# Kernel optimization log

Measured on AMD Instinct MI355X. Metric: run time of the kernel, lower is better.

## Reference

```python
import jax, jax.numpy as jnp
import numpy as np

D_MODEL = 1024
N_LAYERS = 2
D_STATE = 64
D_CONV = 4
EXPAND = 2
D_INNER = EXPAND * D_MODEL            # 2048
HEADDIM = D_STATE                     # 64 (headdim=d_state per module code)
NHEADS = D_INNER // HEADDIM           # 32
CONV_DIM = D_INNER + 2 * D_STATE      # 2176 (ngroups=1)
D_IN_PROJ = 2 * D_INNER + 2 * D_STATE + NHEADS  # 4256
EPS = 1e-5


def setup_inputs() -> dict:
    key = jax.random.key(0)
    ks = jax.random.split(key, 8)
    B, L = 2, 4096
    return {
        "x": jax.random.normal(ks[0], (B, L, D_MODEL), jnp.float32),
        "ln_w": jnp.ones((N_LAYERS, D_MODEL), jnp.float32),
        "ln_b": jnp.zeros((N_LAYERS, D_MODEL), jnp.float32),
        "in_proj_w": jax.random.normal(ks[1], (N_LAYERS, D_IN_PROJ, D_MODEL), jnp.float32) * (D_MODEL ** -0.5),
        "conv_w": jax.random.normal(ks[2], (N_LAYERS, CONV_DIM, D_CONV), jnp.float32) * (D_CONV ** -0.5),
        "conv_b": jnp.zeros((N_LAYERS, CONV_DIM), jnp.float32),
        "dt_bias": jax.random.normal(ks[3], (N_LAYERS, NHEADS), jnp.float32) * 0.5,
        "A_log": jnp.log(jax.random.uniform(ks[4], (N_LAYERS, NHEADS), jnp.float32, 1.0, 16.0)),
        "D": jnp.ones((N_LAYERS, NHEADS), jnp.float32),
        "rms_w": jnp.ones((N_LAYERS, D_INNER), jnp.float32),
        "out_proj_w": jax.random.normal(ks[5], (N_LAYERS, D_MODEL, D_INNER), jnp.float32) * (D_INNER ** -0.5),
    }


def _layernorm(x, w, b):
    m = x.mean(-1, keepdims=True)
    v = ((x - m) ** 2).mean(-1, keepdims=True)
    return (x - m) * jax.lax.rsqrt(v + EPS) * w + b


def _mamba2(u, in_w, conv_w, conv_b, dt_bias, A_log, Dp, rms_w, out_w):
    b, l, _ = u.shape
    zxbcdt = u @ in_w.T                                   # (b,l,D_IN_PROJ)
    z, xBC, dt = jnp.split(zxbcdt, [D_INNER, D_INNER + CONV_DIM], axis=-1)
    dt = jax.nn.softplus(dt + dt_bias)                    # (b,l,H)
    # causal depthwise conv over sequence
    xBC = jnp.transpose(xBC, (0, 2, 1))                   # (b,C,l)
    xBC = jax.lax.conv_general_dilated(
        xBC, conv_w[:, None, :], (1,), [(D_CONV - 1, 0)],
        dimension_numbers=("NCH", "OIH", "NCH"), feature_group_count=CONV_DIM)
    xBC = jnp.transpose(xBC, (0, 2, 1)) + conv_b
    xBC = jax.nn.silu(xBC)
    xh, Bm, Cm = jnp.split(xBC, [D_INNER, D_INNER + D_STATE], axis=-1)
    xh = xh.reshape(b, l, NHEADS, HEADDIM)                # (b,l,H,P)
    A = -jnp.exp(A_log)                                   # (H,)
    dA = jnp.exp(dt * A)                                  # (b,l,H)

    def step(state, inputs):
        dA_t, dt_t, x_t, B_t, C_t = inputs                # (b,H),(b,H),(b,H,P),(b,N),(b,N)
        state = dA_t[:, :, None, None] * state + (dt_t[:, :, None] * x_t)[..., None] * B_t[:, None, None, :]
        y_t = jnp.einsum("bhpn,bn->bhp", state, C_t)
        return state, y_t

    xs = (jnp.moveaxis(dA, 1, 0), jnp.moveaxis(dt, 1, 0), jnp.moveaxis(xh, 1, 0),
          jnp.moveaxis(Bm, 1, 0), jnp.moveaxis(Cm, 1, 0))
    init = jnp.zeros((b, NHEADS, HEADDIM, D_STATE), u.dtype)
    _, ys = jax.lax.scan(step, init, xs)                  # ys: (l,b,H,P)
    y = jnp.moveaxis(ys, 0, 1) + Dp[None, None, :, None] * xh
    y = y.reshape(b, l, D_INNER)
    # gated RMSNorm (norm_before_gate=False): gate then rmsnorm
    y = y * jax.nn.silu(z)
    y = y * jax.lax.rsqrt(jnp.mean(y * y, -1, keepdims=True) + EPS) * rms_w
    return y @ out_w.T


def reference(x, ln_w, ln_b, in_proj_w, conv_w, conv_b, dt_bias, A_log, D, rms_w, out_proj_w):
    h = x
    for i in range(N_LAYERS):
        res = h
        h = _layernorm(h, ln_w[i], ln_b[i])
        h = _mamba2(h, in_proj_w[i], conv_w[i], conv_b[i], dt_bias[i], A_log[i], D[i], rms_w[i], out_proj_w[i])
        h = h + res
    return h
```

## Files before the change

### kernel.cpp

```cpp
#include <hip/hip_runtime.h>
#include <stdint.h>

#define D_MODEL   1024
#define D_STATE   64
#define D_INNER   2048
#define NHEADS    32
#define CONV_DIM  2176
#define D_IN_PROJ 4256
#define NPAD1     4352
#define LSEQ      4096
#define BL        8192
#define NCHUNK    32
#define TCH       128
#define EPS       1e-5f

typedef __attribute__((ext_vector_type(8))) _Float16 f16x8;
typedef __attribute__((ext_vector_type(4))) _Float16 f16x4;
typedef __attribute__((ext_vector_type(4))) float f32x4;

__device__ __forceinline__ void load_lds16(const void* g, void* l) {
  __builtin_amdgcn_global_load_lds((const __attribute__((address_space(1))) void*)g,
                                   (__attribute__((address_space(3))) void*)l, 16, 0, 0);
}

__global__ __launch_bounds__(256) void cvt_w1_kernel(const float* __restrict__ w,
                                                     _Float16* __restrict__ o) {
  size_t idx = (size_t)blockIdx.x * 256 + threadIdx.x;
  int k = idx & 1023;
  size_t nr = idx >> 10;
  int layer = (int)(nr / NPAD1);
  int n = (int)(nr % NPAD1);
  float v = (n < D_IN_PROJ) ? w[((size_t)layer * D_IN_PROJ + n) * 1024 + k] : 0.f;
  o[idx] = (_Float16)v;
}
__global__ __launch_bounds__(256) void cvt_w2_kernel(const float* __restrict__ w,
                                                     _Float16* __restrict__ o) {
  size_t idx = (size_t)blockIdx.x * 256 + threadIdx.x;
  o[idx] = (_Float16)w[idx];
}

__global__ __launch_bounds__(256) void ln_kernel(const float* __restrict__ x,
                                                 const float* __restrict__ w,
                                                 const float* __restrict__ b,
                                                 _Float16* __restrict__ o) {
  int row = blockIdx.x, tid = threadIdx.x;
  const float* xr = x + (size_t)row * D_MODEL;
  float4 v = *(const float4*)(xr + tid * 4);
  float s = v.x + v.y + v.z + v.w;
  float q = v.x * v.x + v.y * v.y + v.z * v.z + v.w * v.w;
  for (int off = 1; off < 64; off <<= 1) { s += __shfl_xor(s, off); q += __shfl_xor(q, off); }
  __shared__ float rs[4], rq[4];
  int wave = tid >> 6, lane = tid & 63;
  if (lane == 0) { rs[wave] = s; rq[wave] = q; }
  __syncthreads();
  s = rs[0] + rs[1] + rs[2] + rs[3];
  q = rq[0] + rq[1] + rq[2] + rq[3];
  float mean = s * (1.f / D_MODEL);
  float var = q * (1.f / D_MODEL) - mean * mean;
  float rstd = rsqrtf(var + EPS);
  int c = tid * 4;
  f16x4 ov;
  ov[0] = (_Float16)((v.x - mean) * rstd * w[c + 0] + b[c + 0]);
  ov[1] = (_Float16)((v.y - mean) * rstd * w[c + 1] + b[c + 1]);
  ov[2] = (_Float16)((v.z - mean) * rstd * w[c + 2] + b[c + 2]);
  ov[3] = (_Float16)((v.w - mean) * rstd * w[c + 3] + b[c + 3]);
  *(f16x4*)(o + (size_t)row * D_MODEL + c) = ov;
}

template <int MODE>
__global__ __launch_bounds__(512, 4) void gemm_f16_kernel(
    const _Float16* __restrict__ A, int lda,
    const _Float16* __restrict__ Bw, int K, int NBN,
    _Float16* __restrict__ Zb, _Float16* __restrict__ XPRE, float* __restrict__ AUX,
    float* __restrict__ Cf, const float* __restrict__ resid) {
  __shared__ _Float16 lA[3][256 * 32];
  __shared__ _Float16 lB[3][128 * 32];
  int tid = threadIdx.x;
  int wv = tid >> 6, lane = tid & 63;
  int nwg = gridDim.x;
  int cpx = nwg >> 3;
  int wg = ((int)blockIdx.x & 7) * cpx + ((int)blockIdx.x >> 3);
  int band = wg / (4 * NBN), rem = wg % (4 * NBN);
  int bm = band * 4 + (rem & 3);
  int bn = rem >> 2;

  const int wm = (wv >> 1) * 64, wn = (wv & 1) * 64;
  const int fr = lane & 15;
  const int s4 = lane >> 4;
  size_t aoff = (size_t)(bm * 256) * lda;
  size_t boff = (size_t)(bn * 128) * K;

  f32x4 acc[4][4];
  f32x4 zero = {0.f, 0.f, 0.f, 0.f};
#pragma unroll
  for (int i = 0; i < 4; ++i)
#pragma unroll
    for (int j = 0; j < 4; ++j) acc[i][j] = zero;

  auto stage = [&](int k0, int buf) {
#pragma unroll
    for (int c = 0; c < 2; ++c) {
      int row = (wv * 2 + c) * 16 + (lane >> 2);
      int col = k0 + (((lane & 3) ^ ((row >> 1) & 3)) << 3);
      load_lds16(A + aoff + (size_t)row * lda + col,
                 &lA[buf][(wv * 2 + c) * 512 + lane * 8]);
    }
    int rowb = wv * 16 + (lane >> 2);
    int colb = k0 + (((lane & 3) ^ ((rowb >> 1) & 3)) << 3);
    load_lds16(Bw + boff + (size_t)rowb * K + colb, &lB[buf][wv * 512 + lane * 8]);
  };

  int nk = K >> 5;
  stage(0, 0);
  stage(32, 1);
  int cur = 0;
  for (int kk = 0; kk < nk; ++kk) {
    if (kk + 2 < nk) {
      int sb = cur + 2; if (sb >= 3) sb -= 3;
      stage((kk + 2) << 5, sb);
      asm volatile("s_waitcnt vmcnt(6)" ::: "memory");
    } else if (kk + 1 < nk) {
      asm volatile("s_waitcnt vmcnt(3)" ::: "memory");
    } else {
      asm volatile("s_waitcnt vmcnt(0)" ::: "memory");
    }
    __builtin_amdgcn_s_barrier();
    __builtin_amdgcn_sched_barrier(0);
    f16x8 af[4], bf[4];
#pragma unroll
    for (int i = 0; i < 4; ++i) {
      int R = wm + i * 16 + fr;
      af[i] = *(const f16x8*)&lA[cur][R * 32 + ((s4 ^ ((R >> 1) & 3)) << 3)];
    }
#pragma unroll
    for (int j = 0; j < 4; ++j) {
      int R = wn + j * 16 + fr;
      bf[j] = *(const f16x8*)&lB[cur][R * 32 + ((s4 ^ ((R >> 1) & 3)) << 3)];
    }
#pragma unroll
    for (int i = 0; i < 4; ++i)
#pragma unroll
      for (int j = 0; j < 4; ++j)
        acc[i][j] = __builtin_amdgcn_mfma_f32_16x16x32_f16(af[i], bf[j], acc[i][j], 0, 0, 0);
    __builtin_amdgcn_sched_barrier(0);
    __builtin_amdgcn_s_barrier();
    cur = cur + 1; if (cur >= 3) cur = 0;
  }

  int r0 = (lane >> 4) * 4;
  int cc = lane & 15;
#pragma unroll
  for (int i = 0; i < 4; ++i) {
#pragma unroll
    for (int j = 0; j < 4; ++j) {
      int col = bn * 128 + wn + j * 16 + cc;
#pragma unroll
      for (int r = 0; r < 4; ++r) {
        size_t row = (size_t)(bm * 256 + wm + i * 16 + r0 + r);
        float v = acc[i][j][r];
        if constexpr (MODE == 0) {
          if (col < 2048)       Zb[row * 2048 + col] = (_Float16)v;
          else if (col < 4096)  XPRE[row * 2048 + (col - 2048)] = (_Float16)v;
          else if (col < 4256)  AUX[row * 160 + (col - 4096)] = v;
        } else {
          size_t idx = row * 1024 + col;
          Cf[idx] = v + resid[idx];
        }
      }
    }
  }
}

__global__ __launch_bounds__(128) void dtlc_kernel(const float* __restrict__ aux,
                                                   const float* __restrict__ dtb,
                                                   const float* __restrict__ alog,
                                                   float* __restrict__ dtt,
                                                   float* __restrict__ lco) {
  int bid = blockIdx.x;
  int h = bid >> 6, b = (bid >> 5) & 1, ct = bid & 31;
  int tid = threadIdx.x, lane = tid & 63;
  int l = b * LSEQ + ct * TCH + tid;
  float A = -__expf(alog[h]);
  float v = aux[(size_t)l * 160 + 128 + h] + dtb[h];
  float sp = (v > 20.f) ? v : log1pf(expf(v));
  size_t base = (size_t)h * BL + b * LSEQ + ct * TCH;
  dtt[base + tid] = sp;
  float d = sp * A;
#pragma unroll
  for (int off = 1; off < 64; off <<= 1) {
    float o = __shfl_up(d, off);
    if (lane >= off) d += o;
  }
  __shared__ float tot;
  if (tid == 63) tot = d;
  __syncthreads();
  if (tid >= 64) d += tot;
  lco[base + tid] = d;
}

__global__ __launch_bounds__(256) void conv_kernel(const _Float16* __restrict__ xpre,
                                                   const float* __restrict__ aux,
                                                   const float* __restrict__ cw,
                                                   const float* __restrict__ cb,
                                                   _Float16* __restrict__ xh,
                                                   float* __restrict__ Bo,
                                                   float* __restrict__ Co) {
  int c = blockIdx.y * 256 + threadIdx.x;
  if (c >= CONV_DIM) return;
  int l0 = blockIdx.x * 16;
  float w0 = cw[c * 4 + 0], w1 = cw[c * 4 + 1], w2 = cw[c * 4 + 2], w3 = cw[c * 4 + 3];
  float bias = cb[c];
  bool isx = (c < 2048);
  auto ldx = [&](int l) -> float {
    return isx ? (float)xpre[(size_t)l * 2048 + c] : aux[(size_t)l * 160 + (c - 2048)];
  };
  float a0 = 0.f, a1 = 0.f, a2 = 0.f;
  if ((l0 & 4095) != 0) { a0 = ldx(l0 - 3); a1 = ldx(l0 - 2); a2 = ldx(l0 - 1); }
#pragma unroll
  for (int t = 0; t < 16; ++t) {
    int l = l0 + t;
    float a3 = ldx(l);
    float acc = bias + a0 * w0 + a1 * w1 + a2 * w2 + a3 * w3;
    acc = acc / (1.f + __expf(-acc));
    if (isx)
      xh[(size_t)l * 2048 + c] = (_Float16)acc;
    else if (c < 2112)
      Bo[(size_t)l * 64 + (c - 2048)] = acc;
    else
      Co[(size_t)l * 64 + (c - 2112)] = acc;
    a0 = a1; a1 = a2; a2 = a3;
  }
}

__global__ __launch_bounds__(256) void transpose_x_kernel(const _Float16* __restrict__ xh,
                                                          _Float16* __restrict__ xt) {
  __shared__ _Float16 T[64 * 65];
  int c0 = blockIdx.x * 64;
  int l0 = blockIdx.y * 64;
  int tid = threadIdx.x;
  int rr = tid >> 3, g8 = tid & 7;
#pragma unroll
  for (int p = 0; p < 2; ++p) {
    int l = p * 32 + rr;
    f16x8 v = *(const f16x8*)&xh[(size_t)(l0 + l) * 2048 + c0 + g8 * 8];
#pragma unroll
    for (int j = 0; j < 8; ++j) T[l * 65 + g8 * 8 + j] = v[j];
  }
  __syncthreads();
#pragma unroll
  for (int p = 0; p < 2; ++p) {
    int c = p * 32 + rr;
    f16x8 v;
#pragma unroll
    for (int j = 0; j < 8; ++j) v[j] = T[(g8 * 8 + j) * 65 + c];
    *(f16x8*)&xt[(size_t)(c0 + c) * 8192 + l0 + g8 * 8] = v;
  }
}

__global__ __launch_bounds__(256) void transpose_b_kernel(const float* __restrict__ bc,
                                                          _Float16* __restrict__ bt) {
  __shared__ _Float16 T[64 * 65];
  int l0 = blockIdx.x * 64;
  int tid = threadIdx.x;
  int rr4 = tid >> 4, cl = tid & 15;
#pragma unroll
  for (int p = 0; p < 4; ++p) {
    int l = p * 16 + rr4;
    float4 v = *(const float4*)&bc[(size_t)(l0 + l) * 64 + cl * 4];
    T[l * 65 + cl * 4 + 0] = (_Float16)v.x;
    T[l * 65 + cl * 4 + 1] = (_Float16)v.y;
    T[l * 65 + cl * 4 + 2] = (_Float16)v.z;
    T[l * 65 + cl * 4 + 3] = (_Float16)v.w;
  }
  __syncthreads();
  int rr = tid >> 3, g8 = tid & 7;
#pragma unroll
  for (int p = 0; p < 2; ++p) {
    int n = p * 32 + rr;
    f16x8 v;
#pragma unroll
    for (int j = 0; j < 8; ++j) v[j] = T[(g8 * 8 + j) * 65 + n];
    *(f16x8*)&bt[(size_t)n * 8192 + l0 + g8 * 8] = v;
  }
}

__global__ __launch_bounds__(256) void scan_state_kernel(
    const _Float16* __restrict__ xt, const _Float16* __restrict__ bt,
    const float* __restrict__ lc, const float* __restrict__ dtt,
    float* __restrict__ cs) {
  int bid = blockIdx.x;
  int chunk = bid & 31, h = (bid >> 5) & 31, b = bid >> 10;
  int tid = threadIdx.x;
  size_t gb = (size_t)b * LSEQ + chunk * TCH;
  size_t cdb = (size_t)h * BL + gb;
  __shared__ _Float16 xtl[64 * 128];
  __shared__ _Float16 btl[64 * 128];
  __shared__ float ldsW[128];
  if (tid < 128) ldsW[tid] = dtt[cdb + tid] * __expf(lc[cdb + 127] - lc[cdb + tid]);
  __syncthreads();
  int rr = tid >> 4, cl = tid & 15;
#pragma unroll
  for (int p = 0; p < 4; ++p) {
    int row = p * 16 + rr;
    f16x8 v = *(const f16x8*)&xt[(size_t)(h * 64 + row) * BL + gb + cl * 8];
    f16x8 bv = *(const f16x8*)&bt[(size_t)row * BL + gb + cl * 8];
    f16x8 sv;
#pragma unroll
    for (int j = 0; j < 8; ++j) sv[j] = (_Float16)((float)v[j] * ldsW[cl * 8 + j]);
    int byo = (row * 256 + cl * 16) ^ ((row & 7) << 4);
    *(f16x8*)((char*)xtl + byo) = sv;
    *(f16x8*)((char*)btl + byo) = bv;
  }
  __syncthreads();
  int wv = tid >> 6, lane = tid & 63;
  int fr = lane & 15, fk = (lane >> 4) * 8, r0 = (lane >> 4) * 4, cc = lane & 15;
  int swz = (fr & 7) << 4;
  f32x4 acc[4];
  f32x4 zero = {0.f, 0.f, 0.f, 0.f};
#pragma unroll
  for (int j = 0; j < 4; ++j) acc[j] = zero;
#pragma unroll
  for (int k0 = 0; k0 < 128; k0 += 32) {
    f16x8 af = *(const f16x8*)((char*)xtl + (((wv * 16 + fr) * 256 + (k0 + fk) * 2) ^ swz));
#pragma unroll
    for (int j = 0; j < 4; ++j) {
      f16x8 bf = *(const f16x8*)((char*)btl + (((j * 16 + fr) * 256 + (k0 + fk) * 2) ^ swz));
      acc[j] = __builtin_amdgcn_mfma_f32_16x16x32_f16(af, bf, acc[j], 0, 0, 0);
    }
  }
  size_t cbase = (((size_t)(b * 32 + h) * 32) + chunk) * 4096;
#pragma unroll
  for (int j = 0; j < 4; ++j)
#pragma unroll
    for (int r = 0; r < 4; ++r)
      cs[cbase + (wv * 16 + r0 + r) * 64 + j * 16 + cc] = acc[j][r];
}

__global__ __launch_bounds__(256) void scan_p2_kernel(float* __restrict__ cs,
                                                      const float* __restrict__ lc) {
  int bid = blockIdx.x;
  int b = bid >> 7, h = (bid >> 2) & 31, pq = bid & 3;
  int tid = threadIdx.x;
  size_t base = ((size_t)(b * 32 + h) * 32) * 4096 + (size_t)(pq * 256 + tid) * 4;
  const float* lcd = lc + (size_t)h * BL + b * LSEQ;
  float4 s = {0.f, 0.f, 0.f, 0.f};
  for (int c = 0; c < NCHUNK; ++c) {
    size_t idx = base + (size_t)c * 4096;
    float4 e = *(const float4*)&cs[idx];
    float P = __expf(lcd[c * TCH + TCH - 1]);
    *(float4*)&cs[idx] = s;
    s.x = e.x + P * s.x;
    s.y = e.y + P * s.y;
    s.z = e.z + P * s.z;
    s.w = e.w + P * s.w;
  }
}

__global__ __launch_bounds__(256) void scan_y_kernel(
    const _Float16* __restrict__ xt, const float* __restrict__ Cc,
    const float* __restrict__ Bc, const float* __restrict__ cs,
    const float* __restrict__ lc, const float* __restrict__ dtt,
    const float* __restrict__ Dv, float* __restrict__ y) {
  int bid = blockIdx.x;
  int chunk = bid & 31, h = (bid >> 5) & 31, b = bid >> 10;
  int tid = threadIdx.x;
  size_t gb = (size_t)b * LSEQ + chunk * TCH;
  size_t cdb = (size_t)h * BL + gb;

  __shared__ _Float16 uCB[2 * 128 * 64];
  __shared__ _Float16 xtl[64 * 128];
  __shared__ _Float16 spl[64 * 64];
  __shared__ float ldsLc[128];
  __shared__ float ldsDt[128];
  _Float16* Cl = uCB;
  _Float16* Bl = uCB + 128 * 64;
  _Float16* Pl = uCB;

  int rr = tid >> 4, cl = tid & 15;
#pragma unroll
  for (int p = 0; p < 8; ++p) {
    int row = p * 16 + rr;
    float4 cv = *(const float4*)&Cc[(gb + row) * 64 + cl * 4];
    float4 bv = *(const float4*)&Bc[(gb + row) * 64 + cl * 4];
    f16x4 ch = {(_Float16)cv.x, (_Float16)cv.y, (_Float16)cv.z, (_Float16)cv.w};
    f16x4 bh = {(_Float16)bv.x, (_Float16)bv.y, (_Float16)bv.z, (_Float16)bv.w};
    int byo = (row * 128 + cl * 8) ^ ((row & 7) << 4);
    *(f16x4*)((char*)Cl + byo) = ch;
    *(f16x4*)((char*)Bl + byo) = bh;
  }
  size_t cbase = (((size_t)(b * 32 + h) * 32) + chunk) * 4096;
#pragma unroll
  for (int p = 0; p < 4; ++p) {
    int row = p * 16 + rr;
    f16x8 v = *(const f16x8*)&xt[(size_t)(h * 64 + row) * BL + gb + cl * 8];
    int byo = (row * 256 + cl * 16) ^ ((row & 7) << 4);
    *(f16x8*)((char*)xtl + byo) = v;
    float4 sv = *(const float4*)&cs[cbase + row * 64 + cl * 4];
    f16x4 sh = {(_Float16)sv.x, (_Float16)sv.y, (_Float16)sv.z, (_Float16)sv.w};
    int byo2 = (row * 128 + cl * 8) ^ ((row & 7) << 4);
    *(f16x4*)((char*)spl + byo2) = sh;
  }
  if (tid < 128) { ldsLc[tid] = lc[cdb + tid]; ldsDt[tid] = dtt[cdb + tid]; }
  __syncthreads();

  int wv = tid >> 6, lane = tid & 63;
  int fr = lane & 15, fk = (lane >> 4) * 8, r0 = (lane >> 4) * 4, cc = lane & 15;
  int tb = wv * 32;
  int swz = (fr & 7) << 4;

  f32x4 accY[2][4];
  f32x4 accS[2][8];
  f32x4 zero = {0.f, 0.f, 0.f, 0.f};
#pragma unroll
  for (int i = 0; i < 2; ++i) {
#pragma unroll
    for (int j = 0; j < 4; ++j) accY[i][j] = zero;
#pragma unroll
    for (int j = 0; j < 8; ++j) accS[i][j] = zero;
  }

#pragma unroll
  for (int k0 = 0; k0 < 64; k0 += 32) {
    f16x8 ac[2];
#pragma unroll
    for (int i = 0; i < 2; ++i)
      ac[i] = *(const f16x8*)((char*)Cl + (((tb + i * 16 + fr) * 128 + (k0 + fk) * 2) ^ swz));
#pragma unroll
    for (int j = 0; j < 4; ++j) {
      f16x8 bs = *(const f16x8*)((char*)spl + (((j * 16 + fr) * 128 + (k0 + fk) * 2) ^ swz));
#pragma unroll
      for (int i = 0; i < 2; ++i)
        accY[i][j] = __builtin_amdgcn_mfma_f32_16x16x32_f16(ac[i], bs, accY[i][j], 0, 0, 0);
    }
#pragma unroll
    for (int j = 0; j < 8; ++j) {
      f16x8 bb = *(const f16x8*)((char*)Bl + (((j * 16 + fr) * 128 + (k0 + fk) * 2) ^ swz));
#pragma unroll
      for (int i = 0; i < 2; ++i)
        accS[i][j] = __builtin_amdgcn_mfma_f32_16x16x32_f16(ac[i], bb, accS[i][j], 0, 0, 0);
    }
  }

  float lct[2][4];
#pragma unroll
  for (int i = 0; i < 2; ++i)
#pragma unroll
    for (int r = 0; r < 4; ++r) lct[i][r] = ldsLc[tb + i * 16 + r0 + r];
#pragma unroll
  for (int i = 0; i < 2; ++i)
#pragma unroll
    for (int r = 0; r < 4; ++r) {
      float sc = __expf(lct[i][r]);
#pragma unroll
      for (int j = 0; j < 4; ++j) accY[i][j][r] *= sc;
    }

  __syncthreads();
  float Dh = Dv[h];
#pragma unroll
  for (int i = 0; i < 2; ++i)
#pragma unroll
    for (int jj = 0; jj < 8; ++jj) {
      int s = jj * 16 + cc;
      float lcs = ldsLc[s];
      float dts = ldsDt[s];
#pragma unroll
      for (int r = 0; r < 4; ++r) {
        int t = tb + i * 16 + r0 + r;
        float v = 0.f;
        if (s <= t) v = accS[i][jj][r] * __expf(lct[i][r] - lcs) * dts;
        if (s == t) v += Dh;
        int byo = (t * 256 + s * 2) ^ ((t & 7) << 4);
        *(_Float16*)((char*)Pl + byo) = (_Float16)v;
      }
    }
  __syncthreads();

#pragma unroll
  for (int k0 = 0; k0 < 128; k0 += 32) {
    f16x8 ap[2];
#pragma unroll
    for (int i = 0; i < 2; ++i)
      ap[i] = *(const f16x8*)((char*)Pl + (((tb + i * 16 + fr) * 256 + (k0 + fk) * 2) ^ swz));
#pragma unroll
    for (int j = 0; j < 4; ++j) {
      f16x8 bx = *(const f16x8*)((char*)xtl + (((j * 16 + fr) * 256 + (k0 + fk) * 2) ^ swz));
#pragma unroll
      for (int i = 0; i < 2; ++i)
        accY[i][j] = __builtin_amdgcn_mfma_f32_16x16x32_f16(ap[i], bx, accY[i][j], 0, 0, 0);
    }
  }

#pragma unroll
  for (int i = 0; i < 2; ++i)
#pragma unroll
    for (int j = 0; j < 4; ++j)
#pragma unroll
      for (int r = 0; r < 4; ++r) {
        int t = tb + i * 16 + r0 + r;
        y[(gb + t) * 2048 + h * 64 + j * 16 + cc] = accY[i][j][r];
      }
}

__global__ __launch_bounds__(256) void gate_rms_kernel(const float* __restrict__ yf,
                                                       const _Float16* __restrict__ zb,
                                                       const float* __restrict__ rw,
                                                       _Float16* __restrict__ g) {
  int row = blockIdx.x, tid = threadIdx.x;
  const float* yr = yf + (size_t)row * D_INNER;
  const _Float16* zr = zb + (size_t)row * D_INNER;
  float gv[8];
  float q = 0.f;
#pragma unroll
  for (int u = 0; u < 8; ++u) {
    int c = u * 256 + tid;
    float yv = yr[c];
    float zv = (float)zr[c];
    float t = yv * (zv / (1.f + __expf(-zv)));
    gv[u] = t;
    q += t * t;
  }
  for (int off = 1; off < 64; off <<= 1) q += __shfl_xor(q, off);
  __shared__ float rq[4];
  if ((tid & 63) == 0) rq[tid >> 6] = q;
  __syncthreads();
  q = rq[0] + rq[1] + rq[2] + rq[3];
  float scale = rsqrtf(q * (1.f / D_INNER) + EPS);
  _Float16* gr = g + (size_t)row * D_INNER;
#pragma unroll
  for (int u = 0; u < 8; ++u) {
    int c = u * 256 + tid;
    gr[c] = (_Float16)(gv[u] * scale * rw[c]);
  }
}

extern "C" void kernel_launch(void* const* d_in, const int* in_sizes, int n_in,
                              void* d_out, int out_size, void* d_ws, size_t ws_size,
                              hipStream_t stream) {
  (void)in_sizes; (void)n_in; (void)out_size; (void)ws_size;
  const float* x     = (const float*)d_in[0];
  const float* ln_w  = (const float*)d_in[1];
  const float* ln_b  = (const float*)d_in[2];
  const float* w_in  = (const float*)d_in[3];
  const float* cw    = (const float*)d_in[4];
  const float* cb    = (const float*)d_in[5];
  const float* dtb   = (const float*)d_in[6];
  const float* alog  = (const float*)d_in[7];
  const float* dvec  = (const float*)d_in[8];
  const float* rmsw  = (const float*)d_in[9];
  const float* w_out = (const float*)d_in[10];
  float* out = (float*)d_out;

  char* ws = (char*)d_ws;
  size_t off = 0;
  auto alloc = [&](size_t bytes) -> char* {
    char* p = ws + off;
    off += (bytes + 255) & ~(size_t)255;
    return p;
  };
  _Float16* W1 = (_Float16*)alloc(2ull * 2 * NPAD1 * 1024);
  _Float16* W2 = (_Float16*)alloc(2ull * 2 * 1024 * 2048);
  char* REGION = alloc(4ull * BL * D_INNER);
  _Float16* LNf = (_Float16*)REGION;
  float* Yf = (float*)REGION;
  _Float16* Zb = (_Float16*)alloc(2ull * BL * D_INNER);
  _Float16* XPRE = (_Float16*)alloc(2ull * BL * D_INNER);
  _Float16* XT = XPRE;
  _Float16* XH = (_Float16*)alloc(2ull * BL * D_INNER);
  float* AUX  = (float*)alloc(4ull * BL * 160);
  float* BC = (float*)alloc(4ull * BL * D_STATE);
  float* CC = (float*)alloc(4ull * BL * D_STATE);
  float* DTt = (float*)alloc(4ull * NHEADS * BL);
  float* LC  = (float*)alloc(4ull * NHEADS * BL);
  _Float16* BT = (_Float16*)alloc(2ull * D_STATE * BL);
  float* CS = (float*)alloc(4ull * 2 * NHEADS * NCHUNK * 4096);

  cvt_w1_kernel<<<(2 * NPAD1 * 1024) / 256, 256, 0, stream>>>(w_in, W1);
  cvt_w2_kernel<<<(2 * 1024 * 2048) / 256, 256, 0, stream>>>(w_out, W2);

  for (int layer = 0; layer < 2; ++layer) {
    const float* hin = layer ? (const float*)out : x;
    size_t o1 = (size_t)layer * NPAD1 * 1024;
    size_t o2 = (size_t)layer * 1024 * 2048;
    ln_kernel<<<BL, 256, 0, stream>>>(hin, ln_w + layer * D_MODEL, ln_b + layer * D_MODEL, LNf);
    gemm_f16_kernel<0><<<dim3((8192 / 256) * (NPAD1 / 128)), 512, 0, stream>>>(
        LNf, 1024, W1 + o1, 1024, NPAD1 / 128, Zb, XPRE, AUX, nullptr, nullptr);
    dtlc_kernel<<<2048, 128, 0, stream>>>(AUX, dtb + layer * NHEADS,
                                          alog + layer * NHEADS, DTt, LC);
    conv_kernel<<<dim3(BL / 16, 9), 256, 0, stream>>>(XPRE, AUX, cw + layer * CONV_DIM * 4,
                                                      cb + layer * CONV_DIM, XH, BC, CC);
    transpose_x_kernel<<<dim3(32, 128), 256, 0, stream>>>(XH, XT);
    transpose_b_kernel<<<128, 256, 0, stream>>>(BC, BT);
    scan_state_kernel<<<2048, 256, 0, stream>>>(XT, BT, LC, DTt, CS);
    scan_p2_kernel<<<256, 256, 0, stream>>>(CS, LC);
    scan_y_kernel<<<2048, 256, 0, stream>>>(XT, CC, BC, CS, LC, DTt,
                                            dvec + layer * NHEADS, Yf);
    gate_rms_kernel<<<BL, 256, 0, stream>>>(Yf, Zb, rmsw + layer * D_INNER, Zb);
    gemm_f16_kernel<1><<<dim3((8192 / 256) * (1024 / 128)), 512, 0, stream>>>(
        Zb, 2048, W2 + o2, 2048, 1024 / 128, nullptr, nullptr, nullptr, out, hin);
  }
}
```

Baseline: 783.3 us.

## Enlarge GEMM tiles to 256x256 with 4-stage pipeline and split-phase MFMA

The GEMM block tile grows from 256x128 to 256x256, with each wave computing a 128x64 sub-tile (8x4 accumulators). The LDS ring goes from 3 to 4 buffers, and prefetch runs 3 k-steps ahead. A and B staging is interleaved with two half-MFMA phases under s_setprio. The goal is more data reuse per loaded byte and better overlap of loads with MFMA. The cost is more registers and LDS (launch bounds drop to 2 waves/SIMD) and fewer workgroups (544 and 128 blocks), which may hurt occupancy and tail balance, especially for the out-projection GEMM.

Result: slower. 804.8 us (+2.7%).

```diff
diff --git a/kernel.cpp b/kernel.cpp
--- a/kernel.cpp
+++ b/kernel.cpp
@@ -68,92 +68,122 @@
 }
 
 template <int MODE>
-__global__ __launch_bounds__(512, 4) void gemm_f16_kernel(
+__global__ __launch_bounds__(512, 2) void gemm_f16_kernel(
     const _Float16* __restrict__ A, int lda,
     const _Float16* __restrict__ Bw, int K, int NBN,
     _Float16* __restrict__ Zb, _Float16* __restrict__ XPRE, float* __restrict__ AUX,
     float* __restrict__ Cf, const float* __restrict__ resid) {
-  __shared__ _Float16 lA[3][256 * 32];
-  __shared__ _Float16 lB[3][128 * 32];
+  __shared__ _Float16 lA[4][256 * 32];
+  __shared__ _Float16 lB[4][256 * 32];
   int tid = threadIdx.x;
   int wv = tid >> 6, lane = tid & 63;
   int nwg = gridDim.x;
   int cpx = nwg >> 3;
   int wg = ((int)blockIdx.x & 7) * cpx + ((int)blockIdx.x >> 3);
-  int band = wg / (4 * NBN), rem = wg % (4 * NBN);
-  int bm = band * 4 + (rem & 3);
-  int bn = rem >> 2;
-
-  const int wm = (wv >> 1) * 64, wn = (wv & 1) * 64;
+  int bm = wg / NBN, bn = wg % NBN;
+
+  const int wm = (wv >> 2) * 128;
+  const int wn = (wv & 3) * 64;
   const int fr = lane & 15;
   const int s4 = lane >> 4;
   size_t aoff = (size_t)(bm * 256) * lda;
-  size_t boff = (size_t)(bn * 128) * K;
-
-  f32x4 acc[4][4];
+  size_t boff = (size_t)(bn * 256) * K;
+
+  const int srow = tid >> 2;
+  const int sslot = tid & 3;
+
+  f32x4 acc[8][4];
   f32x4 zero = {0.f, 0.f, 0.f, 0.f};
 #pragma unroll
-  for (int i = 0; i < 4; ++i)
+  for (int i = 0; i < 8; ++i)
 #pragma unroll
     for (int j = 0; j < 4; ++j) acc[i][j] = zero;
 
-  auto stage = [&](int k0, int buf) {
-#pragma unroll
-    for (int c = 0; c < 2; ++c) {
-      int row = (wv * 2 + c) * 16 + (lane >> 2);
-      int col = k0 + (((lane & 3) ^ ((row >> 1) & 3)) << 3);
-      load_lds16(A + aoff + (size_t)row * lda + col,
-                 &lA[buf][(wv * 2 + c) * 512 + lane * 8]);
-    }
-    int rowb = wv * 16 + (lane >> 2);
-    int colb = k0 + (((lane & 3) ^ ((rowb >> 1) & 3)) << 3);
-    load_lds16(Bw + boff + (size_t)rowb * K + colb, &lB[buf][wv * 512 + lane * 8]);
+  auto stageA = [&](int kt, int buf) {
+#pragma unroll
+    for (int rr = 0; rr < 2; ++rr) {
+      int row = rr * 128 + srow;
+      int col = kt * 32 + ((sslot ^ ((row >> 1) & 3)) << 3);
+      load_lds16(A + aoff + (size_t)row * lda + col, &lA[buf][row * 32 + sslot * 8]);
+    }
   };
+  auto stageB = [&](int kt, int buf) {
+#pragma unroll
+    for (int rr = 0; rr < 2; ++rr) {
+      int row = rr * 128 + srow;
+      int col = kt * 32 + ((sslot ^ ((row >> 1) & 3)) << 3);
+      load_lds16(Bw + boff + (size_t)row * K + col, &lB[buf][row * 32 + sslot * 8]);
+    }
+  };
 
   int nk = K >> 5;
-  stage(0, 0);
-  stage(32, 1);
-  int cur = 0;
-  for (int kk = 0; kk < nk; ++kk) {
-    if (kk + 2 < nk) {
-      int sb = cur + 2; if (sb >= 3) sb -= 3;
-      stage((kk + 2) << 5, sb);
-      asm volatile("s_waitcnt vmcnt(6)" ::: "memory");
-    } else if (kk + 1 < nk) {
-      asm volatile("s_waitcnt vmcnt(3)" ::: "memory");
-    } else {
-      asm volatile("s_waitcnt vmcnt(0)" ::: "memory");
-    }
-    __builtin_amdgcn_s_barrier();
-    __builtin_amdgcn_sched_barrier(0);
+  stageA(0, 0); stageB(0, 0);
+  stageA(1, 1); stageB(1, 1);
+  stageA(2, 2); stageB(2, 2);
+  asm volatile("s_waitcnt vmcnt(8)" ::: "memory");
+  __builtin_amdgcn_s_barrier();
+
+  for (int t = 0; t < nk; ++t) {
+    int buf = t & 3;
+    int pbuf = (t + 3) & 3;
+    bool pf = (t + 3 < nk);
     f16x8 af[4], bf[4];
+#pragma unroll
+    for (int j = 0; j < 4; ++j) {
+      int R = wn + j * 16 + fr;
+      bf[j] = *(const f16x8*)&lB[buf][R * 32 + ((s4 ^ ((R >> 1) & 3)) << 3)];
+    }
 #pragma unroll
     for (int i = 0; i < 4; ++i) {
       int R = wm + i * 16 + fr;
-      af[i] = *(const f16x8*)&lA[cur][R * 32 + ((s4 ^ ((R >> 1) & 3)) << 3)];
-    }
-#pragma unroll
-    for (int j = 0; j < 4; ++j) {
-      int R = wn + j * 16 + fr;
-      bf[j] = *(const f16x8*)&lB[cur][R * 32 + ((s4 ^ ((R >> 1) & 3)) << 3)];
-    }
+      af[i] = *(const f16x8*)&lA[buf][R * 32 + ((s4 ^ ((R >> 1) & 3)) << 3)];
+    }
+    if (pf) stageA(t + 3, pbuf);
+    __builtin_amdgcn_s_barrier();
+    asm volatile("s_waitcnt lgkmcnt(0)" ::: "memory");
+    __builtin_amdgcn_sched_barrier(0);
+    __builtin_amdgcn_s_setprio(1);
 #pragma unroll
     for (int i = 0; i < 4; ++i)
 #pragma unroll
       for (int j = 0; j < 4; ++j)
         acc[i][j] = __builtin_amdgcn_mfma_f32_16x16x32_f16(af[i], bf[j], acc[i][j], 0, 0, 0);
+    __builtin_amdgcn_s_setprio(0);
     __builtin_amdgcn_sched_barrier(0);
     __builtin_amdgcn_s_barrier();
-    cur = cur + 1; if (cur >= 3) cur = 0;
+#pragma unroll
+    for (int i = 0; i < 4; ++i) {
+      int R = wm + 64 + i * 16 + fr;
+      af[i] = *(const f16x8*)&lA[buf][R * 32 + ((s4 ^ ((R >> 1) & 3)) << 3)];
+    }
+    if (pf) stageB(t + 3, pbuf);
+    if (t + 1 < nk) {
+      int rem = nk - 2 - t;
+      if (rem >= 2)      asm volatile("s_waitcnt vmcnt(8)" ::: "memory");
+      else if (rem == 1) asm volatile("s_waitcnt vmcnt(4)" ::: "memory");
+      else               asm volatile("s_waitcnt vmcnt(0)" ::: "memory");
+    }
+    __builtin_amdgcn_s_barrier();
+    asm volatile("s_waitcnt lgkmcnt(0)" ::: "memory");
+    __builtin_amdgcn_sched_barrier(0);
+    __builtin_amdgcn_s_setprio(1);
+#pragma unroll
+    for (int i = 0; i < 4; ++i)
+#pragma unroll
+      for (int j = 0; j < 4; ++j)
+        acc[4 + i][j] = __builtin_amdgcn_mfma_f32_16x16x32_f16(af[i], bf[j], acc[4 + i][j], 0, 0, 0);
+    __builtin_amdgcn_s_setprio(0);
+    __builtin_amdgcn_sched_barrier(0);
+    __builtin_amdgcn_s_barrier();
   }
 
   int r0 = (lane >> 4) * 4;
   int cc = lane & 15;
 #pragma unroll
-  for (int i = 0; i < 4; ++i) {
+  for (int i = 0; i < 8; ++i) {
 #pragma unroll
     for (int j = 0; j < 4; ++j) {
-      int col = bn * 128 + wn + j * 16 + cc;
+      int col = bn * 256 + wn + j * 16 + cc;
 #pragma unroll
       for (int r = 0; r < 4; ++r) {
         size_t row = (size_t)(bm * 256 + wm + i * 16 + r0 + r);
@@ -583,8 +613,8 @@
     size_t o1 = (size_t)layer * NPAD1 * 1024;
     size_t o2 = (size_t)layer * 1024 * 2048;
     ln_kernel<<<BL, 256, 0, stream>>>(hin, ln_w + layer * D_MODEL, ln_b + layer * D_MODEL, LNf);
-    gemm_f16_kernel<0><<<dim3((8192 / 256) * (NPAD1 / 128)), 512, 0, stream>>>(
-        LNf, 1024, W1 + o1, 1024, NPAD1 / 128, Zb, XPRE, AUX, nullptr, nullptr);
+    gemm_f16_kernel<0><<<dim3((8192 / 256) * (NPAD1 / 256)), 512, 0, stream>>>(
+        LNf, 1024, W1 + o1, 1024, NPAD1 / 256, Zb, XPRE, AUX, nullptr, nullptr);
     dtlc_kernel<<<2048, 128, 0, stream>>>(AUX, dtb + layer * NHEADS,
                                           alog + layer * NHEADS, DTt, LC);
     conv_kernel<<<dim3(BL / 16, 9), 256, 0, stream>>>(XPRE, AUX, cw + layer * CONV_DIM * 4,
@@ -596,7 +626,7 @@
     scan_y_kernel<<<2048, 256, 0, stream>>>(XT, CC, BC, CS, LC, DTt,
                                             dvec + layer * NHEADS, Yf);
     gate_rms_kernel<<<BL, 256, 0, stream>>>(Yf, Zb, rmsw + layer * D_INNER, Zb);
-    gemm_f16_kernel<1><<<dim3((8192 / 256) * (1024 / 128)), 512, 0, stream>>>(
-        Zb, 2048, W2 + o2, 2048, 1024 / 128, nullptr, nullptr, nullptr, out, hin);
-  }
-}
+    gemm_f16_kernel<1><<<dim3((8192 / 256) * (1024 / 256)), 512, 0, stream>>>(
+        Zb, 2048, W2 + o2, 2048, 1024 / 256, nullptr, nullptr, nullptr, out, hin);
+  }
+}
```

## Fuse transposes into conv, store y in fp16, vectorize gate RMS

Applied to the files above, without the earlier changes.

The conv kernel now writes x and B directly in channel-major (transposed) layout using 16-byte stores, so the two separate transpose kernels and the XH buffer are no longer needed. The scan output y is stored as fp16 instead of fp32, which halves that write and the matching read in the gate/RMS kernel. The gate/RMS kernel now uses vectorized 8-element loads and stores per thread. The cost is lower precision on y and per-thread strided column writes from the conv kernel, which may coalesce worse than the old tiled transposes.

Result: faster. 743.7 us (-5.1%).

```diff
diff --git a/kernel.cpp b/kernel.cpp
--- a/kernel.cpp
+++ b/kernel.cpp
@@ -202,9 +202,10 @@
                                                    const float* __restrict__ aux,
                                                    const float* __restrict__ cw,
                                                    const float* __restrict__ cb,
-                                                   _Float16* __restrict__ xh,
+                                                   _Float16* __restrict__ xt,
                                                    float* __restrict__ Bo,
-                                                   float* __restrict__ Co) {
+                                                   float* __restrict__ Co,
+                                                   _Float16* __restrict__ bt) {
   int c = blockIdx.y * 256 + threadIdx.x;
   if (c >= CONV_DIM) return;
   int l0 = blockIdx.x * 16;
@@ -216,71 +217,29 @@
   };
   float a0 = 0.f, a1 = 0.f, a2 = 0.f;
   if ((l0 & 4095) != 0) { a0 = ldx(l0 - 3); a1 = ldx(l0 - 2); a2 = ldx(l0 - 1); }
+  _Float16 ob[16];
 #pragma unroll
   for (int t = 0; t < 16; ++t) {
     int l = l0 + t;
     float a3 = ldx(l);
     float acc = bias + a0 * w0 + a1 * w1 + a2 * w2 + a3 * w3;
     acc = acc / (1.f + __expf(-acc));
-    if (isx)
-      xh[(size_t)l * 2048 + c] = (_Float16)acc;
-    else if (c < 2112)
-      Bo[(size_t)l * 64 + (c - 2048)] = acc;
-    else
-      Co[(size_t)l * 64 + (c - 2112)] = acc;
+    ob[t] = (_Float16)acc;
+    if (!isx) {
+      if (c < 2112) Bo[(size_t)l * 64 + (c - 2048)] = acc;
+      else          Co[(size_t)l * 64 + (c - 2112)] = acc;
+    }
     a0 = a1; a1 = a2; a2 = a3;
   }
-}
-
-__global__ __launch_bounds__(256) void transpose_x_kernel(const _Float16* __restrict__ xh,
-                                                          _Float16* __restrict__ xt) {
-  __shared__ _Float16 T[64 * 65];
-  int c0 = blockIdx.x * 64;
-  int l0 = blockIdx.y * 64;
-  int tid = threadIdx.x;
-  int rr = tid >> 3, g8 = tid & 7;
-#pragma unroll
-  for (int p = 0; p < 2; ++p) {
-    int l = p * 32 + rr;
-    f16x8 v = *(const f16x8*)&xh[(size_t)(l0 + l) * 2048 + c0 + g8 * 8];
-#pragma unroll
-    for (int j = 0; j < 8; ++j) T[l * 65 + g8 * 8 + j] = v[j];
-  }
-  __syncthreads();
-#pragma unroll
-  for (int p = 0; p < 2; ++p) {
-    int c = p * 32 + rr;
-    f16x8 v;
-#pragma unroll
-    for (int j = 0; j < 8; ++j) v[j] = T[(g8 * 8 + j) * 65 + c];
-    *(f16x8*)&xt[(size_t)(c0 + c) * 8192 + l0 + g8 * 8] = v;
-  }
-}
-
-__global__ __launch_bounds__(256) void transpose_b_kernel(const float* __restrict__ bc,
-                                                          _Float16* __restrict__ bt) {
-  __shared__ _Float16 T[64 * 65];
-  int l0 = blockIdx.x * 64;
-  int tid = threadIdx.x;
-  int rr4 = tid >> 4, cl = tid & 15;
-#pragma unroll
-  for (int p = 0; p < 4; ++p) {
-    int l = p * 16 + rr4;
-    float4 v = *(const float4*)&bc[(size_t)(l0 + l) * 64 + cl * 4];
-    T[l * 65 + cl * 4 + 0] = (_Float16)v.x;
-    T[l * 65 + cl * 4 + 1] = (_Float16)v.y;
-    T[l * 65 + cl * 4 + 2] = (_Float16)v.z;
-    T[l * 65 + cl * 4 + 3] = (_Float16)v.w;
-  }
-  __syncthreads();
-  int rr = tid >> 3, g8 = tid & 7;
-#pragma unroll
-  for (int p = 0; p < 2; ++p) {
-    int n = p * 32 + rr;
-    f16x8 v;
-#pragma unroll
-    for (int j = 0; j < 8; ++j) v[j] = T[(g8 * 8 + j) * 65 + n];
-    *(f16x8*)&bt[(size_t)n * 8192 + l0 + g8 * 8] = v;
+  f16x8 v0, v1;
+#pragma unroll
+  for (int j = 0; j < 8; ++j) { v0[j] = ob[j]; v1[j] = ob[8 + j]; }
+  if (isx) {
+    *(f16x8*)&xt[(size_t)c * 8192 + l0] = v0;
+    *(f16x8*)&xt[(size_t)c * 8192 + l0 + 8] = v1;
+  } else if (c < 2112) {
+    *(f16x8*)&bt[(size_t)(c - 2048) * 8192 + l0] = v0;
+    *(f16x8*)&bt[(size_t)(c - 2048) * 8192 + l0 + 8] = v1;
   }
 }
 
@@ -360,7 +319,7 @@
     const _Float16* __restrict__ xt, const float* __restrict__ Cc,
     const float* __restrict__ Bc, const float* __restrict__ cs,
     const float* __restrict__ lc, const float* __restrict__ dtt,
-    const float* __restrict__ Dv, float* __restrict__ y) {
+    const float* __restrict__ Dv, _Float16* __restrict__ y) {
   int bid = blockIdx.x;
   int chunk = bid & 31, h = (bid >> 5) & 31, b = bid >> 10;
   int tid = threadIdx.x;
@@ -498,25 +457,25 @@
 #pragma unroll
       for (int r = 0; r < 4; ++r) {
         int t = tb + i * 16 + r0 + r;
-        y[(gb + t) * 2048 + h * 64 + j * 16 + cc] = accY[i][j][r];
+        y[(gb + t) * 2048 + h * 64 + j * 16 + cc] = (_Float16)accY[i][j][r];
       }
 }
 
-__global__ __launch_bounds__(256) void gate_rms_kernel(const float* __restrict__ yf,
+__global__ __launch_bounds__(256) void gate_rms_kernel(const _Float16* __restrict__ yf,
                                                        const _Float16* __restrict__ zb,
                                                        const float* __restrict__ rw,
                                                        _Float16* __restrict__ g) {
   int row = blockIdx.x, tid = threadIdx.x;
-  const float* yr = yf + (size_t)row * D_INNER;
-  const _Float16* zr = zb + (size_t)row * D_INNER;
+  int c0 = tid * 8;
+  f16x8 yv = *(const f16x8*)(yf + (size_t)row * D_INNER + c0);
+  f16x8 zv = *(const f16x8*)(zb + (size_t)row * D_INNER + c0);
   float gv[8];
   float q = 0.f;
 #pragma unroll
   for (int u = 0; u < 8; ++u) {
-    int c = u * 256 + tid;
-    float yv = yr[c];
-    float zv = (float)zr[c];
-    float t = yv * (zv / (1.f + __expf(-zv)));
+    float yy = (float)yv[u];
+    float zz = (float)zv[u];
+    float t = yy * (zz / (1.f + __expf(-zz)));
     gv[u] = t;
     q += t * t;
   }
@@ -526,12 +485,18 @@
   __syncthreads();
   q = rq[0] + rq[1] + rq[2] + rq[3];
   float scale = rsqrtf(q * (1.f / D_INNER) + EPS);
-  _Float16* gr = g + (size_t)row * D_INNER;
-#pragma unroll
-  for (int u = 0; u < 8; ++u) {
-    int c = u * 256 + tid;
-    gr[c] = (_Float16)(gv[u] * scale * rw[c]);
-  }
+  float4 r0 = *(const float4*)&rw[c0];
+  float4 r1 = *(const float4*)&rw[c0 + 4];
+  f16x8 o;
+  o[0] = (_Float16)(gv[0] * scale * r0.x);
+  o[1] = (_Float16)(gv[1] * scale * r0.y);
+  o[2] = (_Float16)(gv[2] * scale * r0.z);
+  o[3] = (_Float16)(gv[3] * scale * r0.w);
+  o[4] = (_Float16)(gv[4] * scale * r1.x);
+  o[5] = (_Float16)(gv[5] * scale * r1.y);
+  o[6] = (_Float16)(gv[6] * scale * r1.z);
+  o[7] = (_Float16)(gv[7] * scale * r1.w);
+  *(f16x8*)(g + (size_t)row * D_INNER + c0) = o;
 }
 
 extern "C" void kernel_launch(void* const* d_in, const int* in_sizes, int n_in,
@@ -562,11 +527,10 @@
   _Float16* W2 = (_Float16*)alloc(2ull * 2 * 1024 * 2048);
   char* REGION = alloc(4ull * BL * D_INNER);
   _Float16* LNf = (_Float16*)REGION;
-  float* Yf = (float*)REGION;
+  _Float16* Yf = (_Float16*)REGION;
   _Float16* Zb = (_Float16*)alloc(2ull * BL * D_INNER);
   _Float16* XPRE = (_Float16*)alloc(2ull * BL * D_INNER);
-  _Float16* XT = XPRE;
-  _Float16* XH = (_Float16*)alloc(2ull * BL * D_INNER);
+  _Float16* XT = (_Float16*)alloc(2ull * BL * D_INNER);
   float* AUX  = (float*)alloc(4ull * BL * 160);
   float* BC = (float*)alloc(4ull * BL * D_STATE);
   float* CC = (float*)alloc(4ull * BL * D_STATE);
@@ -588,9 +552,7 @@
     dtlc_kernel<<<2048, 128, 0, stream>>>(AUX, dtb + layer * NHEADS,
                                           alog + layer * NHEADS, DTt, LC);
     conv_kernel<<<dim3(BL / 16, 9), 256, 0, stream>>>(XPRE, AUX, cw + layer * CONV_DIM * 4,
-                                                      cb + layer * CONV_DIM, XH, BC, CC);
-    transpose_x_kernel<<<dim3(32, 128), 256, 0, stream>>>(XH, XT);
-    transpose_b_kernel<<<128, 256, 0, stream>>>(BC, BT);
+                                                      cb + layer * CONV_DIM, XT, BC, CC, BT);
     scan_state_kernel<<<2048, 256, 0, stream>>>(XT, BT, LC, DTt, CS);
     scan_p2_kernel<<<256, 256, 0, stream>>>(CS, LC);
     scan_y_kernel<<<2048, 256, 0, stream>>>(XT, CC, BC, CS, LC, DTt,
```
